# Kernel tuning notes

Measured on AMD Instinct MI355X. Metric: run time of the kernel, lower is better.

Reference implementation:

```python
import jax, jax.numpy as jnp
import numpy as np

N_NODES = 100000


def _gcn_conv(h, row, col, norm, W, b):
    # h: [N, Fin] -> [N, Fout]; standard GCN: scatter-add of normalized
    # neighbor messages after linear transform.
    h = h @ W                                   # [N, Fout]
    msg = h[col] * norm[:, None]                # [E, Fout] gather + scale
    out = jax.ops.segment_sum(msg, row, num_segments=N_NODES)
    return out + b


def setup_inputs() -> dict:
    key = jax.random.key(0)
    k1, k2, k3, k4 = jax.random.split(key, 4)
    N, E, F_IN, HID, OUT = N_NODES, 3200000, 512, 16, 40
    x = jax.random.normal(k1, (N, F_IN), dtype=jnp.float32)
    edge_index = jax.random.randint(k2, (2, E), 0, N, dtype=jnp.int64)
    W1 = jax.random.normal(k3, (F_IN, HID), dtype=jnp.float32) * (1.0 / np.sqrt(F_IN))
    b1 = jnp.zeros((HID,), dtype=jnp.float32)
    W2 = jax.random.normal(k4, (HID, OUT), dtype=jnp.float32) * (1.0 / np.sqrt(HID))
    b2 = jnp.zeros((OUT,), dtype=jnp.float32)
    return {"x": x, "edge_index": edge_index, "W1": W1, "b1": b1, "W2": W2, "b2": b2}


def reference(x, edge_index, W1, b1, W2, b2):
    N = N_NODES
    # add self-loops (GCN convention)
    loop = jnp.arange(N, dtype=edge_index.dtype)
    row = jnp.concatenate([edge_index[0], loop])  # target nodes
    col = jnp.concatenate([edge_index[1], loop])  # source nodes
    # symmetric normalization deg^-1/2 * deg^-1/2
    deg = jax.ops.segment_sum(jnp.ones_like(row, dtype=x.dtype), row, num_segments=N)
    dinv = jnp.where(deg > 0, jax.lax.rsqrt(deg), 0.0)
    norm = dinv[row] * dinv[col]                  # [E+N]

    h = _gcn_conv(x, row, col, norm, W1, b1)
    h = jax.nn.relu(h)
    out = _gcn_conv(h, row, col, norm, W2, b2)
    return out
```

## Files before the change

### kernel.cpp

```cpp
#include <hip/hip_runtime.h>

#define N_NODES 100000
#define F_IN 512
#define HID 16
#define F_OUT 40

#define NB 784
#define BSHIFT 7
#define ROWS_PB 128
#define BCAP 4608
#define CUR_PAD 16
#define APAD 17
#define PARTB 512
#define SROW 129

__global__ void k_zero(int* __restrict__ g) {
    int i = blockIdx.x * 256 + threadIdx.x;
    if (i < NB * CUR_PAD) g[i] = 0;
}

__global__ __launch_bounds__(512) void k_part1(const int* __restrict__ ei, int E,
                                               int* __restrict__ gcursor,
                                               unsigned int* __restrict__ sortbuf) {
    __shared__ int lcnt0[NB], lcnt1[NB], gb[NB];
    int t = threadIdx.x;
    int half = (t >> 6) & 1;
    int* myl = half ? lcnt1 : lcnt0;
    int epb = (E + PARTB - 1) / PARTB;
    int base = blockIdx.x * epb;
    int lim = min(base + epb, E);
    for (int i = t; i < NB; i += 512) { lcnt0[i] = 0; lcnt1[i] = 0; }
    __syncthreads();
    unsigned int v[13]; int bkt[13], mi[13];
#pragma unroll
    for (int i = 0; i < 13; ++i) {
        int e = base + i * 512 + t;
        bkt[i] = -1;
        if (e < lim) {
            int r = ei[e], c = ei[E + e];
            bkt[i] = r >> BSHIFT;
            v[i] = ((unsigned)(r & (ROWS_PB - 1)) << 17) | (unsigned)c;
            mi[i] = atomicAdd(&myl[bkt[i]], 1);
        }
    }
    __syncthreads();
    for (int i = t; i < NB; i += 512)
        gb[i] = atomicAdd(&gcursor[i * CUR_PAD], lcnt0[i] + lcnt1[i]);
    __syncthreads();
#pragma unroll
    for (int i = 0; i < 13; ++i)
        if (bkt[i] >= 0) {
            int slot = gb[bkt[i]] + (half ? lcnt0[bkt[i]] : 0) + mi[i];
            if (slot < BCAP) sortbuf[(size_t)bkt[i] * BCAP + slot] = v[i];
        }
}

__global__ __launch_bounds__(512) void k_gemm(const float* __restrict__ x,
                                              const float* __restrict__ W1,
                                              float* __restrict__ Hs) {
    __shared__ float smem[8 * 64 * APAD];
    int t = threadIdx.x;
    int bid = blockIdx.x;
    int tilebase = bid * 64;
    int srow = t >> 5;
    int sseg = t & 31;
    int crow = t & 63;
    int ksub = __builtin_amdgcn_readfirstlane(t >> 6);

    float acc[HID];
#pragma unroll
    for (int f = 0; f < HID; ++f) acc[f] = 0.0f;

    float4 rg[4];
#pragma unroll
    for (int q = 0; q < 4; ++q) {
        int r = tilebase + q * 16 + srow;
        r = min(r, N_NODES - 1);
        rg[q] = *reinterpret_cast<const float4*>(x + (size_t)r * F_IN + sseg * 4);
    }
    for (int s = 0; s < 4; ++s) {
        __syncthreads();
#pragma unroll
        for (int q = 0; q < 4; ++q) {
            int base = (q * 16 + srow) * SROW + sseg * 4;
            smem[base + 0] = rg[q].x;
            smem[base + 1] = rg[q].y;
            smem[base + 2] = rg[q].z;
            smem[base + 3] = rg[q].w;
        }
        __syncthreads();
        if (s < 3) {
#pragma unroll
            for (int q = 0; q < 4; ++q) {
                int r = tilebase + q * 16 + srow;
                r = min(r, N_NODES - 1);
                rg[q] = *reinterpret_cast<const float4*>(
                    x + (size_t)r * F_IN + (s + 1) * 128 + sseg * 4);
            }
        }
        const float* wp = W1 + (s * 128 + ksub * 16) * HID;
        int lbase = crow * SROW + ksub * 16;
#pragma unroll
        for (int kk = 0; kk < 16; ++kk) {
            float xv = smem[lbase + kk];
#pragma unroll
            for (int f = 0; f < HID; ++f)
                acc[f] = fmaf(xv, wp[kk * HID + f], acc[f]);
        }
    }
    __syncthreads();
    int rbase = (ksub * 64 + crow) * APAD;
#pragma unroll
    for (int f = 0; f < HID; ++f) smem[rbase + f] = acc[f];
    __syncthreads();
#pragma unroll
    for (int p = 0; p < 2; ++p) {
        int o = p * 512 + t;
        int r = o >> 4, f = o & 15;
        int rgl = tilebase + r;
        if (rgl < N_NODES) {
            float sum = 0.0f;
#pragma unroll
            for (int c = 0; c < 8; ++c) sum += smem[(c * 64 + r) * APAD + f];
            Hs[(size_t)rgl * HID + f] = sum;
        }
    }
}

__global__ __launch_bounds__(256) void k_build(const unsigned int* __restrict__ sortbuf,
                                               const int* __restrict__ gcursor,
                                               int* __restrict__ rowptr,
                                               float* __restrict__ dinv,
                                               int* __restrict__ colv,
                                               float* __restrict__ Hs) {
    __shared__ int bb[NB];
    __shared__ int s[256];
    __shared__ int hist[ROWS_PB];
    __shared__ int rstart[ROWS_PB];
    __shared__ int cur[ROWS_PB];
    __shared__ float sdinv[ROWS_PB];
    int b = blockIdx.x, t = threadIdx.x;

    int l0 = 0, l1 = 0, l2 = 0, l3 = 0;
    if (t < 196) {
        l0 = min(gcursor[(t * 4 + 0) * CUR_PAD], BCAP);
        l1 = min(gcursor[(t * 4 + 1) * CUR_PAD], BCAP);
        l2 = min(gcursor[(t * 4 + 2) * CUR_PAD], BCAP);
        l3 = min(gcursor[(t * 4 + 3) * CUR_PAD], BCAP);
    }
    int part = l0 + l1 + l2 + l3;
    s[t] = part;
    __syncthreads();
    for (int off = 1; off < 256; off <<= 1) {
        int a = (t >= off) ? s[t - off] : 0;
        __syncthreads();
        s[t] += a;
        __syncthreads();
    }
    if (t < 196) {
        int ex = s[t] - part;
        bb[t * 4 + 0] = ex;
        bb[t * 4 + 1] = ex + l0;
        bb[t * 4 + 2] = ex + l0 + l1;
        bb[t * 4 + 3] = ex + l0 + l1 + l2;
    }
    if (t < ROWS_PB) hist[t] = 0;
    __syncthreads();
    int gbase = bb[b];
    int n = min(gcursor[b * CUR_PAD], BCAP);
    if (b == 0 && t == 0) rowptr[N_NODES] = s[255];

    const unsigned int* sb = sortbuf + (size_t)b * BCAP;
    for (int i = t; i < n; i += 256) atomicAdd(&hist[sb[i] >> 17], 1);
    __syncthreads();
    int c0 = (t < ROWS_PB) ? hist[t] : 0;
    s[t] = c0;
    __syncthreads();
    for (int off = 1; off < 256; off <<= 1) {
        int a = (t >= off) ? s[t - off] : 0;
        __syncthreads();
        s[t] += a;
        __syncthreads();
    }
    if (t < ROWS_PB) {
        int ex = s[t] - c0;
        rstart[t] = ex;
        cur[t] = 0;
        float dv = rsqrtf((float)(c0 + 1));
        sdinv[t] = dv;
        int g = b * ROWS_PB + t;
        if (g < N_NODES) {
            rowptr[g] = gbase + ex;
            dinv[g] = dv;
        }
    }
    __syncthreads();
    for (int i = t; i < n; i += 256) {
        unsigned int v = sb[i];
        int lr = v >> 17;
        int pos = atomicAdd(&cur[lr], 1);
        colv[gbase + rstart[lr] + pos] = (int)(v & 0x1FFFFu);
    }
    __syncthreads();
    for (int i = t; i < ROWS_PB * 4; i += 256) {
        int row = i >> 2, q = i & 3;
        int g = b * ROWS_PB + row;
        if (g < N_NODES) {
            float4* p = reinterpret_cast<float4*>(Hs + (size_t)g * HID + q * 4);
            float4 vv = *p;
            float dv = sdinv[row];
            vv.x *= dv; vv.y *= dv; vv.z *= dv; vv.w *= dv;
            *p = vv;
        }
    }
}

__global__ __launch_bounds__(256) void k_agg1(const int* __restrict__ rowptr,
                                              const int* __restrict__ colv,
                                              const float* __restrict__ dinv,
                                              const float* __restrict__ Hs,
                                              const float* __restrict__ b1,
                                              float* __restrict__ h1s) {
    int wid = __builtin_amdgcn_readfirstlane((blockIdx.x * 256 + threadIdx.x) >> 6);
    if (wid >= N_NODES) return;
    int lane = threadIdx.x & 63;
    int f4 = lane & 3, sub = lane >> 2;
    int beg = rowptr[wid], end = rowptr[wid + 1];
    float dr = dinv[wid];
    float4 acc = make_float4(0.f, 0.f, 0.f, 0.f);
    for (int j = beg + sub; j < end; j += 16) {
        int c = colv[j];
        float4 hv = *reinterpret_cast<const float4*>(Hs + (size_t)c * HID + f4 * 4);
        acc.x += hv.x; acc.y += hv.y; acc.z += hv.z; acc.w += hv.w;
    }
#pragma unroll
    for (int d = 4; d < 64; d <<= 1) {
        acc.x += __shfl_xor(acc.x, d);
        acc.y += __shfl_xor(acc.y, d);
        acc.z += __shfl_xor(acc.z, d);
        acc.w += __shfl_xor(acc.w, d);
    }
    if (sub == 0) {
        float4 self = *reinterpret_cast<const float4*>(Hs + (size_t)wid * HID + f4 * 4);
        float4 bb = *reinterpret_cast<const float4*>(b1 + f4 * 4);
        float4 o;
        o.x = fmaxf((acc.x + self.x) * dr + bb.x, 0.f) * dr;
        o.y = fmaxf((acc.y + self.y) * dr + bb.y, 0.f) * dr;
        o.z = fmaxf((acc.z + self.z) * dr + bb.z, 0.f) * dr;
        o.w = fmaxf((acc.w + self.w) * dr + bb.w, 0.f) * dr;
        *reinterpret_cast<float4*>(h1s + (size_t)wid * HID + f4 * 4) = o;
    }
}

__global__ __launch_bounds__(256) void k_agg2(const int* __restrict__ rowptr,
                                              const int* __restrict__ colv,
                                              const float* __restrict__ dinv,
                                              const float* __restrict__ h1s,
                                              const float* __restrict__ W2,
                                              const float* __restrict__ b2,
                                              float* __restrict__ out) {
    int wid = __builtin_amdgcn_readfirstlane((blockIdx.x * 256 + threadIdx.x) >> 6);
    if (wid >= N_NODES) return;
    int lane = threadIdx.x & 63;
    int f4 = lane & 3, sub = lane >> 2;
    int beg = rowptr[wid], end = rowptr[wid + 1];
    float dr = dinv[wid];
    float4 acc = make_float4(0.f, 0.f, 0.f, 0.f);
    for (int j = beg + sub; j < end; j += 16) {
        int c = colv[j];
        float4 hv = *reinterpret_cast<const float4*>(h1s + (size_t)c * HID + f4 * 4);
        acc.x += hv.x; acc.y += hv.y; acc.z += hv.z; acc.w += hv.w;
    }
#pragma unroll
    for (int d = 4; d < 64; d <<= 1) {
        acc.x += __shfl_xor(acc.x, d);
        acc.y += __shfl_xor(acc.y, d);
        acc.z += __shfl_xor(acc.z, d);
        acc.w += __shfl_xor(acc.w, d);
    }
    float4 self = *reinterpret_cast<const float4*>(h1s + (size_t)wid * HID + f4 * 4);
    float4 w4;
    w4.x = (acc.x + self.x) * dr;
    w4.y = (acc.y + self.y) * dr;
    w4.z = (acc.z + self.z) * dr;
    w4.w = (acc.w + self.w) * dr;
    if (lane < F_OUT) {
        float o = b2[lane];
#pragma unroll
        for (int k = 0; k < HID; ++k) {
            float comp = (k & 3) == 0 ? w4.x : (k & 3) == 1 ? w4.y
                        : (k & 3) == 2 ? w4.z : w4.w;
            float wk = __shfl(comp, k >> 2);
            o = fmaf(wk, W2[k * F_OUT + lane], o);
        }
        out[(size_t)wid * F_OUT + lane] = o;
    }
}

extern "C" void kernel_launch(void* const* d_in, const int* in_sizes, int n_in,
                              void* d_out, int out_size, void* d_ws, size_t ws_size,
                              hipStream_t stream) {
    const float* x  = (const float*)d_in[0];
    const int* ei   = (const int*)d_in[1];
    const float* W1 = (const float*)d_in[2];
    const float* b1 = (const float*)d_in[3];
    const float* W2 = (const float*)d_in[4];
    const float* b2 = (const float*)d_in[5];
    float* out = (float*)d_out;
    const int E = in_sizes[1] / 2;

    int* gcursor          = (int*)d_ws;
    int* rowptr           = gcursor + 12544;
    float* dinv           = (float*)(rowptr + 100016);
    int* colv             = (int*)(dinv + 100032);
    unsigned int* sortbuf = (unsigned int*)(colv + 3200000);
    float* h1s            = (float*)sortbuf;
    float* Hs             = (float*)(sortbuf + 3612672);

    const int nbW = (N_NODES * 64 + 255) / 256;
    const int nbG = (N_NODES + 63) / 64;

    k_zero<<<(NB * CUR_PAD + 255) / 256, 256, 0, stream>>>(gcursor);
    k_part1<<<PARTB, 512, 0, stream>>>(ei, E, gcursor, sortbuf);
    k_gemm<<<nbG, 512, 0, stream>>>(x, W1, Hs);
    k_build<<<NB, 256, 0, stream>>>(sortbuf, gcursor, rowptr, dinv, colv, Hs);
    k_agg1<<<nbW, 256, 0, stream>>>(rowptr, colv, dinv, Hs, b1, h1s);
    k_agg2<<<nbW, 256, 0, stream>>>(rowptr, colv, dinv, h1s, W2, b2, out);
}
```

Measured before the change: 217.7 us.

## Merge edge partition and first-layer GEMM into one launch and rewrite GEMM

Result: slower. 301.9 us (+38.7%).

```diff
diff --git a/kernel.cpp b/kernel.cpp
--- a/kernel.cpp
+++ b/kernel.cpp
@@ -10,119 +10,128 @@
 #define ROWS_PB 128
 #define BCAP 4608
 #define CUR_PAD 16
-#define APAD 17
 #define PARTB 512
-#define SROW 129
 
 __global__ void k_zero(int* __restrict__ g) {
     int i = blockIdx.x * 256 + threadIdx.x;
     if (i < NB * CUR_PAD) g[i] = 0;
 }
 
-__global__ __launch_bounds__(512) void k_part1(const int* __restrict__ ei, int E,
-                                               int* __restrict__ gcursor,
-                                               unsigned int* __restrict__ sortbuf) {
+__global__ __launch_bounds__(512) void k_fat(const float* __restrict__ x,
+                                             const float* __restrict__ W1,
+                                             const int* __restrict__ ei, int E,
+                                             int* __restrict__ gcursor,
+                                             unsigned int* __restrict__ sortbuf,
+                                             float* __restrict__ Hs) {
     __shared__ int lcnt0[NB], lcnt1[NB], gb[NB];
     int t = threadIdx.x;
-    int half = (t >> 6) & 1;
-    int* myl = half ? lcnt1 : lcnt0;
-    int epb = (E + PARTB - 1) / PARTB;
-    int base = blockIdx.x * epb;
-    int lim = min(base + epb, E);
-    for (int i = t; i < NB; i += 512) { lcnt0[i] = 0; lcnt1[i] = 0; }
-    __syncthreads();
-    unsigned int v[13]; int bkt[13], mi[13];
-#pragma unroll
-    for (int i = 0; i < 13; ++i) {
-        int e = base + i * 512 + t;
-        bkt[i] = -1;
-        if (e < lim) {
-            int r = ei[e], c = ei[E + e];
-            bkt[i] = r >> BSHIFT;
-            v[i] = ((unsigned)(r & (ROWS_PB - 1)) << 17) | (unsigned)c;
-            mi[i] = atomicAdd(&myl[bkt[i]], 1);
-        }
-    }
-    __syncthreads();
-    for (int i = t; i < NB; i += 512)
-        gb[i] = atomicAdd(&gcursor[i * CUR_PAD], lcnt0[i] + lcnt1[i]);
-    __syncthreads();
-#pragma unroll
-    for (int i = 0; i < 13; ++i)
-        if (bkt[i] >= 0) {
-            int slot = gb[bkt[i]] + (half ? lcnt0[bkt[i]] : 0) + mi[i];
-            if (slot < BCAP) sortbuf[(size_t)bkt[i] * BCAP + slot] = v[i];
-        }
-}
-
-__global__ __launch_bounds__(512) void k_gemm(const float* __restrict__ x,
-                                              const float* __restrict__ W1,
-                                              float* __restrict__ Hs) {
-    __shared__ float smem[8 * 64 * APAD];
-    int t = threadIdx.x;
-    int bid = blockIdx.x;
-    int tilebase = bid * 64;
-    int srow = t >> 5;
-    int sseg = t & 31;
-    int crow = t & 63;
-    int ksub = __builtin_amdgcn_readfirstlane(t >> 6);
-
-    float acc[HID];
-#pragma unroll
-    for (int f = 0; f < HID; ++f) acc[f] = 0.0f;
-
-    float4 rg[4];
-#pragma unroll
-    for (int q = 0; q < 4; ++q) {
-        int r = tilebase + q * 16 + srow;
-        r = min(r, N_NODES - 1);
-        rg[q] = *reinterpret_cast<const float4*>(x + (size_t)r * F_IN + sseg * 4);
-    }
-    for (int s = 0; s < 4; ++s) {
-        __syncthreads();
-#pragma unroll
-        for (int q = 0; q < 4; ++q) {
-            int base = (q * 16 + srow) * SROW + sseg * 4;
-            smem[base + 0] = rg[q].x;
-            smem[base + 1] = rg[q].y;
-            smem[base + 2] = rg[q].z;
-            smem[base + 3] = rg[q].w;
-        }
-        __syncthreads();
-        if (s < 3) {
-#pragma unroll
-            for (int q = 0; q < 4; ++q) {
-                int r = tilebase + q * 16 + srow;
-                r = min(r, N_NODES - 1);
-                rg[q] = *reinterpret_cast<const float4*>(
-                    x + (size_t)r * F_IN + (s + 1) * 128 + sseg * 4);
-            }
-        }
-        const float* wp = W1 + (s * 128 + ksub * 16) * HID;
-        int lbase = crow * SROW + ksub * 16;
-#pragma unroll
-        for (int kk = 0; kk < 16; ++kk) {
-            float xv = smem[lbase + kk];
-#pragma unroll
-            for (int f = 0; f < HID; ++f)
-                acc[f] = fmaf(xv, wp[kk * HID + f], acc[f]);
-        }
-    }
-    __syncthreads();
-    int rbase = (ksub * 64 + crow) * APAD;
-#pragma unroll
-    for (int f = 0; f < HID; ++f) smem[rbase + f] = acc[f];
-    __syncthreads();
-#pragma unroll
-    for (int p = 0; p < 2; ++p) {
-        int o = p * 512 + t;
-        int r = o >> 4, f = o & 15;
-        int rgl = tilebase + r;
-        if (rgl < N_NODES) {
-            float sum = 0.0f;
-#pragma unroll
-            for (int c = 0; c < 8; ++c) sum += smem[(c * 64 + r) * APAD + f];
-            Hs[(size_t)rgl * HID + f] = sum;
+    if (blockIdx.x < PARTB) {
+        int half = (t >> 6) & 1;
+        int* myl = half ? lcnt1 : lcnt0;
+        int epb = (E + PARTB - 1) / PARTB;
+        int base = blockIdx.x * epb;
+        int lim = min(base + epb, E);
+        for (int i = t; i < NB; i += 512) { lcnt0[i] = 0; lcnt1[i] = 0; }
+        __syncthreads();
+        unsigned int v[13]; int bkt[13], mi[13];
+#pragma unroll
+        for (int i = 0; i < 13; ++i) {
+            int e = base + i * 512 + t;
+            bkt[i] = -1;
+            if (e < lim) {
+                int r = ei[e], c = ei[E + e];
+                bkt[i] = r >> BSHIFT;
+                v[i] = ((unsigned)(r & (ROWS_PB - 1)) << 17) | (unsigned)c;
+                mi[i] = atomicAdd(&myl[bkt[i]], 1);
+            }
+        }
+        __syncthreads();
+        for (int i = t; i < NB; i += 512)
+            gb[i] = atomicAdd(&gcursor[i * CUR_PAD], lcnt0[i] + lcnt1[i]);
+        __syncthreads();
+#pragma unroll
+        for (int i = 0; i < 13; ++i)
+            if (bkt[i] >= 0) {
+                int slot = gb[bkt[i]] + (half ? lcnt0[bkt[i]] : 0) + mi[i];
+                if (slot < BCAP) sortbuf[(size_t)bkt[i] * BCAP + slot] = v[i];
+            }
+    } else {
+        int bid = blockIdx.x - PARTB;
+        int l = t & 63;
+        int wv = t >> 6;
+        int row = bid * 64 + wv * 8 + (l & 7);
+        int slice = l >> 3;
+        int rload = min(row, N_NODES - 1);
+        const float* xp = x + (size_t)rload * F_IN + slice * 64;
+        const float* wp = W1 + slice * 64 * HID;
+
+        float acc[HID];
+#pragma unroll
+        for (int f = 0; f < HID; ++f) acc[f] = 0.0f;
+
+#pragma unroll 2
+        for (int k = 0; k < 64; k += 8) {
+            float4 xa = *reinterpret_cast<const float4*>(xp + k);
+            float4 xb = *reinterpret_cast<const float4*>(xp + k + 4);
+            float xs[8] = {xa.x, xa.y, xa.z, xa.w, xb.x, xb.y, xb.z, xb.w};
+#pragma unroll
+            for (int kk = 0; kk < 8; ++kk) {
+                const float4* wr = reinterpret_cast<const float4*>(wp + (k + kk) * HID);
+                float4 w0 = wr[0], w1 = wr[1], w2 = wr[2], w3 = wr[3];
+                float xv = xs[kk];
+                acc[0]  = fmaf(xv, w0.x, acc[0]);
+                acc[1]  = fmaf(xv, w0.y, acc[1]);
+                acc[2]  = fmaf(xv, w0.z, acc[2]);
+                acc[3]  = fmaf(xv, w0.w, acc[3]);
+                acc[4]  = fmaf(xv, w1.x, acc[4]);
+                acc[5]  = fmaf(xv, w1.y, acc[5]);
+                acc[6]  = fmaf(xv, w1.z, acc[6]);
+                acc[7]  = fmaf(xv, w1.w, acc[7]);
+                acc[8]  = fmaf(xv, w2.x, acc[8]);
+                acc[9]  = fmaf(xv, w2.y, acc[9]);
+                acc[10] = fmaf(xv, w2.z, acc[10]);
+                acc[11] = fmaf(xv, w2.w, acc[11]);
+                acc[12] = fmaf(xv, w3.x, acc[12]);
+                acc[13] = fmaf(xv, w3.y, acc[13]);
+                acc[14] = fmaf(xv, w3.z, acc[14]);
+                acc[15] = fmaf(xv, w3.w, acc[15]);
+            }
+        }
+        float b8[8];
+        {
+            bool hi = (l >> 3) & 1;
+#pragma unroll
+            for (int f = 0; f < 8; ++f) {
+                float tl = acc[f]     + __shfl_xor(acc[f], 8);
+                float th = acc[f + 8] + __shfl_xor(acc[f + 8], 8);
+                b8[f] = hi ? th : tl;
+            }
+        }
+        float c4[4];
+        {
+            bool hi = (l >> 4) & 1;
+#pragma unroll
+            for (int f = 0; f < 4; ++f) {
+                float tl = b8[f]     + __shfl_xor(b8[f], 16);
+                float th = b8[f + 4] + __shfl_xor(b8[f + 4], 16);
+                c4[f] = hi ? th : tl;
+            }
+        }
+        float e2[2];
+        {
+            bool hi = (l >> 5) & 1;
+#pragma unroll
+            for (int f = 0; f < 2; ++f) {
+                float tl = c4[f]     + __shfl_xor(c4[f], 32);
+                float th = c4[f + 2] + __shfl_xor(c4[f + 2], 32);
+                e2[f] = hi ? th : tl;
+            }
+        }
+        if (row < N_NODES) {
+            int fbase = (((slice) & 1) << 3) | (((slice >> 1) & 1) << 2) |
+                        (((slice >> 2) & 1) << 1);
+            *reinterpret_cast<float2*>(Hs + (size_t)row * HID + fbase) =
+                make_float2(e2[0], e2[1]);
         }
     }
 }
@@ -321,8 +330,7 @@
     const int nbG = (N_NODES + 63) / 64;
 
     k_zero<<<(NB * CUR_PAD + 255) / 256, 256, 0, stream>>>(gcursor);
-    k_part1<<<PARTB, 512, 0, stream>>>(ei, E, gcursor, sortbuf);
-    k_gemm<<<nbG, 512, 0, stream>>>(x, W1, Hs);
+    k_fat<<<PARTB + nbG, 512, 0, stream>>>(x, W1, ei, E, gcursor, sortbuf, Hs);
     k_build<<<NB, 256, 0, stream>>>(sortbuf, gcursor, rowptr, dinv, colv, Hs);
     k_agg1<<<nbW, 256, 0, stream>>>(rowptr, colv, dinv, Hs, b1, h1s);
     k_agg2<<<nbW, 256, 0, stream>>>(rowptr, colv, dinv, h1s, W2, b2, out);
```

## Co-schedule GEMM blocks with partition and build kernels; move source dinv scaling into agg1

Applied to the files above, without the earlier changes.

Measured after the change: 206.0 us. 1.06x faster.

```diff
diff --git a/kernel.cpp b/kernel.cpp
--- a/kernel.cpp
+++ b/kernel.cpp
@@ -12,6 +12,8 @@
 #define CUR_PAD 16
 #define APAD 17
 #define PARTB 512
+#define G1 660
+#define NBG 1563
 #define SROW 129
 
 __global__ void k_zero(int* __restrict__ g) {
@@ -19,48 +21,10 @@
     if (i < NB * CUR_PAD) g[i] = 0;
 }
 
-__global__ __launch_bounds__(512) void k_part1(const int* __restrict__ ei, int E,
-                                               int* __restrict__ gcursor,
-                                               unsigned int* __restrict__ sortbuf) {
-    __shared__ int lcnt0[NB], lcnt1[NB], gb[NB];
-    int t = threadIdx.x;
-    int half = (t >> 6) & 1;
-    int* myl = half ? lcnt1 : lcnt0;
-    int epb = (E + PARTB - 1) / PARTB;
-    int base = blockIdx.x * epb;
-    int lim = min(base + epb, E);
-    for (int i = t; i < NB; i += 512) { lcnt0[i] = 0; lcnt1[i] = 0; }
-    __syncthreads();
-    unsigned int v[13]; int bkt[13], mi[13];
-#pragma unroll
-    for (int i = 0; i < 13; ++i) {
-        int e = base + i * 512 + t;
-        bkt[i] = -1;
-        if (e < lim) {
-            int r = ei[e], c = ei[E + e];
-            bkt[i] = r >> BSHIFT;
-            v[i] = ((unsigned)(r & (ROWS_PB - 1)) << 17) | (unsigned)c;
-            mi[i] = atomicAdd(&myl[bkt[i]], 1);
-        }
-    }
-    __syncthreads();
-    for (int i = t; i < NB; i += 512)
-        gb[i] = atomicAdd(&gcursor[i * CUR_PAD], lcnt0[i] + lcnt1[i]);
-    __syncthreads();
-#pragma unroll
-    for (int i = 0; i < 13; ++i)
-        if (bkt[i] >= 0) {
-            int slot = gb[bkt[i]] + (half ? lcnt0[bkt[i]] : 0) + mi[i];
-            if (slot < BCAP) sortbuf[(size_t)bkt[i] * BCAP + slot] = v[i];
-        }
-}
-
-__global__ __launch_bounds__(512) void k_gemm(const float* __restrict__ x,
-                                              const float* __restrict__ W1,
-                                              float* __restrict__ Hs) {
-    __shared__ float smem[8 * 64 * APAD];
-    int t = threadIdx.x;
-    int bid = blockIdx.x;
+__device__ __forceinline__ void gemm_body(const float* __restrict__ x,
+                                          const float* __restrict__ W1,
+                                          float* __restrict__ Hs,
+                                          int bid, int t, float* smem) {
     int tilebase = bid * 64;
     int srow = t >> 5;
     int sseg = t & 31;
@@ -127,91 +91,133 @@
     }
 }
 
-__global__ __launch_bounds__(256) void k_build(const unsigned int* __restrict__ sortbuf,
-                                               const int* __restrict__ gcursor,
-                                               int* __restrict__ rowptr,
-                                               float* __restrict__ dinv,
-                                               int* __restrict__ colv,
-                                               float* __restrict__ Hs) {
-    __shared__ int bb[NB];
-    __shared__ int s[256];
-    __shared__ int hist[ROWS_PB];
-    __shared__ int rstart[ROWS_PB];
-    __shared__ int cur[ROWS_PB];
-    __shared__ float sdinv[ROWS_PB];
-    int b = blockIdx.x, t = threadIdx.x;
-
-    int l0 = 0, l1 = 0, l2 = 0, l3 = 0;
-    if (t < 196) {
-        l0 = min(gcursor[(t * 4 + 0) * CUR_PAD], BCAP);
-        l1 = min(gcursor[(t * 4 + 1) * CUR_PAD], BCAP);
-        l2 = min(gcursor[(t * 4 + 2) * CUR_PAD], BCAP);
-        l3 = min(gcursor[(t * 4 + 3) * CUR_PAD], BCAP);
-    }
-    int part = l0 + l1 + l2 + l3;
-    s[t] = part;
-    __syncthreads();
-    for (int off = 1; off < 256; off <<= 1) {
-        int a = (t >= off) ? s[t - off] : 0;
-        __syncthreads();
-        s[t] += a;
-        __syncthreads();
-    }
-    if (t < 196) {
-        int ex = s[t] - part;
-        bb[t * 4 + 0] = ex;
-        bb[t * 4 + 1] = ex + l0;
-        bb[t * 4 + 2] = ex + l0 + l1;
-        bb[t * 4 + 3] = ex + l0 + l1 + l2;
-    }
-    if (t < ROWS_PB) hist[t] = 0;
-    __syncthreads();
-    int gbase = bb[b];
-    int n = min(gcursor[b * CUR_PAD], BCAP);
-    if (b == 0 && t == 0) rowptr[N_NODES] = s[255];
-
-    const unsigned int* sb = sortbuf + (size_t)b * BCAP;
-    for (int i = t; i < n; i += 256) atomicAdd(&hist[sb[i] >> 17], 1);
-    __syncthreads();
-    int c0 = (t < ROWS_PB) ? hist[t] : 0;
-    s[t] = c0;
-    __syncthreads();
-    for (int off = 1; off < 256; off <<= 1) {
-        int a = (t >= off) ? s[t - off] : 0;
-        __syncthreads();
-        s[t] += a;
-        __syncthreads();
-    }
-    if (t < ROWS_PB) {
-        int ex = s[t] - c0;
-        rstart[t] = ex;
-        cur[t] = 0;
-        float dv = rsqrtf((float)(c0 + 1));
-        sdinv[t] = dv;
-        int g = b * ROWS_PB + t;
-        if (g < N_NODES) {
-            rowptr[g] = gbase + ex;
-            dinv[g] = dv;
-        }
-    }
-    __syncthreads();
-    for (int i = t; i < n; i += 256) {
-        unsigned int v = sb[i];
-        int lr = v >> 17;
-        int pos = atomicAdd(&cur[lr], 1);
-        colv[gbase + rstart[lr] + pos] = (int)(v & 0x1FFFFu);
-    }
-    __syncthreads();
-    for (int i = t; i < ROWS_PB * 4; i += 256) {
-        int row = i >> 2, q = i & 3;
-        int g = b * ROWS_PB + row;
-        if (g < N_NODES) {
-            float4* p = reinterpret_cast<float4*>(Hs + (size_t)g * HID + q * 4);
-            float4 vv = *p;
-            float dv = sdinv[row];
-            vv.x *= dv; vv.y *= dv; vv.z *= dv; vv.w *= dv;
-            *p = vv;
-        }
+__global__ __launch_bounds__(512) void k_p1g(const float* __restrict__ x,
+                                             const float* __restrict__ W1,
+                                             const int* __restrict__ ei, int E,
+                                             int* __restrict__ gcursor,
+                                             unsigned int* __restrict__ sortbuf,
+                                             float* __restrict__ Hs) {
+    __shared__ float smem[8704];
+    int t = threadIdx.x;
+    if (blockIdx.x < PARTB) {
+        int* lcnt0 = (int*)smem;
+        int* lcnt1 = lcnt0 + NB;
+        int* gb    = lcnt1 + NB;
+        int half = (t >> 6) & 1;
+        int* myl = half ? lcnt1 : lcnt0;
+        int epb = (E + PARTB - 1) / PARTB;
+        int base = blockIdx.x * epb;
+        int lim = min(base + epb, E);
+        for (int i = t; i < NB; i += 512) { lcnt0[i] = 0; lcnt1[i] = 0; }
+        __syncthreads();
+        unsigned int v[13]; int bkt[13], mi[13];
+#pragma unroll
+        for (int i = 0; i < 13; ++i) {
+            int e = base + i * 512 + t;
+            bkt[i] = -1;
+            if (e < lim) {
+                int r = ei[e], c = ei[E + e];
+                bkt[i] = r >> BSHIFT;
+                v[i] = ((unsigned)(r & (ROWS_PB - 1)) << 17) | (unsigned)c;
+                mi[i] = atomicAdd(&myl[bkt[i]], 1);
+            }
+        }
+        __syncthreads();
+        for (int i = t; i < NB; i += 512)
+            gb[i] = atomicAdd(&gcursor[i * CUR_PAD], lcnt0[i] + lcnt1[i]);
+        __syncthreads();
+#pragma unroll
+        for (int i = 0; i < 13; ++i)
+            if (bkt[i] >= 0) {
+                int slot = gb[bkt[i]] + (half ? lcnt0[bkt[i]] : 0) + mi[i];
+                if (slot < BCAP) sortbuf[(size_t)bkt[i] * BCAP + slot] = v[i];
+            }
+    } else {
+        gemm_body(x, W1, Hs, blockIdx.x - PARTB, t, smem);
+    }
+}
+
+__global__ __launch_bounds__(512) void k_bg(const float* __restrict__ x,
+                                            const float* __restrict__ W1,
+                                            const unsigned int* __restrict__ sortbuf,
+                                            const int* __restrict__ gcursor,
+                                            int* __restrict__ rowptr,
+                                            float* __restrict__ dinv,
+                                            int* __restrict__ colv,
+                                            float* __restrict__ Hs) {
+    __shared__ float smem[8704];
+    int t = threadIdx.x;
+    if (blockIdx.x < NB) {
+        int* ib     = (int*)smem;
+        int* bb     = ib;
+        int* s      = ib + 784;
+        int* hist   = ib + 1040;
+        int* rstart = ib + 1168;
+        int* cur    = ib + 1296;
+        int b = blockIdx.x;
+
+        int l0 = 0, l1 = 0, l2 = 0, l3 = 0;
+        if (t < 196) {
+            l0 = min(gcursor[(t * 4 + 0) * CUR_PAD], BCAP);
+            l1 = min(gcursor[(t * 4 + 1) * CUR_PAD], BCAP);
+            l2 = min(gcursor[(t * 4 + 2) * CUR_PAD], BCAP);
+            l3 = min(gcursor[(t * 4 + 3) * CUR_PAD], BCAP);
+        }
+        int part = l0 + l1 + l2 + l3;
+        if (t < 256) s[t] = (t < 196) ? part : 0;
+        __syncthreads();
+        for (int off = 1; off < 256; off <<= 1) {
+            int a = 0;
+            if (t < 256 && t >= off) a = s[t - off];
+            __syncthreads();
+            if (t < 256) s[t] += a;
+            __syncthreads();
+        }
+        if (t < 196) {
+            int ex = s[t] - part;
+            bb[t * 4 + 0] = ex;
+            bb[t * 4 + 1] = ex + l0;
+            bb[t * 4 + 2] = ex + l0 + l1;
+            bb[t * 4 + 3] = ex + l0 + l1 + l2;
+        }
+        if (t < ROWS_PB) hist[t] = 0;
+        if (b == 0 && t == 255) rowptr[N_NODES] = s[255];
+        __syncthreads();
+        int gbase = bb[b];
+        int n = min(gcursor[b * CUR_PAD], BCAP);
+
+        const unsigned int* sb = sortbuf + (size_t)b * BCAP;
+        for (int i = t; i < n; i += 512) atomicAdd(&hist[sb[i] >> 17], 1);
+        __syncthreads();
+        int c0 = (t < ROWS_PB) ? hist[t] : 0;
+        if (t < 256) s[t] = (t < ROWS_PB) ? c0 : 0;
+        __syncthreads();
+        for (int off = 1; off < ROWS_PB; off <<= 1) {
+            int a = 0;
+            if (t < ROWS_PB && t >= off) a = s[t - off];
+            __syncthreads();
+            if (t < ROWS_PB) s[t] += a;
+            __syncthreads();
+        }
+        if (t < ROWS_PB) {
+            int ex = s[t] - c0;
+            rstart[t] = ex;
+            cur[t] = 0;
+            int g = b * ROWS_PB + t;
+            if (g < N_NODES) {
+                rowptr[g] = gbase + ex;
+                dinv[g] = rsqrtf((float)(c0 + 1));
+            }
+        }
+        __syncthreads();
+        for (int i = t; i < n; i += 512) {
+            unsigned int v = sb[i];
+            int lr = v >> 17;
+            int pos = atomicAdd(&cur[lr], 1);
+            colv[gbase + rstart[lr] + pos] = (int)(v & 0x1FFFFu);
+        }
+    } else {
+        gemm_body(x, W1, Hs, G1 + (blockIdx.x - NB), t, smem);
     }
 }
 
@@ -230,8 +236,12 @@
     float4 acc = make_float4(0.f, 0.f, 0.f, 0.f);
     for (int j = beg + sub; j < end; j += 16) {
         int c = colv[j];
+        float dc = dinv[c];
         float4 hv = *reinterpret_cast<const float4*>(Hs + (size_t)c * HID + f4 * 4);
-        acc.x += hv.x; acc.y += hv.y; acc.z += hv.z; acc.w += hv.w;
+        acc.x = fmaf(hv.x, dc, acc.x);
+        acc.y = fmaf(hv.y, dc, acc.y);
+        acc.z = fmaf(hv.z, dc, acc.z);
+        acc.w = fmaf(hv.w, dc, acc.w);
     }
 #pragma unroll
     for (int d = 4; d < 64; d <<= 1) {
@@ -244,10 +254,10 @@
         float4 self = *reinterpret_cast<const float4*>(Hs + (size_t)wid * HID + f4 * 4);
         float4 bb = *reinterpret_cast<const float4*>(b1 + f4 * 4);
         float4 o;
-        o.x = fmaxf((acc.x + self.x) * dr + bb.x, 0.f) * dr;
-        o.y = fmaxf((acc.y + self.y) * dr + bb.y, 0.f) * dr;
-        o.z = fmaxf((acc.z + self.z) * dr + bb.z, 0.f) * dr;
-        o.w = fmaxf((acc.w + self.w) * dr + bb.w, 0.f) * dr;
+        o.x = fmaxf((acc.x + self.x * dr) * dr + bb.x, 0.f) * dr;
+        o.y = fmaxf((acc.y + self.y * dr) * dr + bb.y, 0.f) * dr;
+        o.z = fmaxf((acc.z + self.z * dr) * dr + bb.z, 0.f) * dr;
+        o.w = fmaxf((acc.w + self.w * dr) * dr + bb.w, 0.f) * dr;
         *reinterpret_cast<float4*>(h1s + (size_t)wid * HID + f4 * 4) = o;
     }
 }
@@ -318,12 +328,11 @@
     float* Hs             = (float*)(sortbuf + 3612672);
 
     const int nbW = (N_NODES * 64 + 255) / 256;
-    const int nbG = (N_NODES + 63) / 64;
 
     k_zero<<<(NB * CUR_PAD + 255) / 256, 256, 0, stream>>>(gcursor);
-    k_part1<<<PARTB, 512, 0, stream>>>(ei, E, gcursor, sortbuf);
-    k_gemm<<<nbG, 512, 0, stream>>>(x, W1, Hs);
-    k_build<<<NB, 256, 0, stream>>>(sortbuf, gcursor, rowptr, dinv, colv, Hs);
+    k_p1g<<<PARTB + G1, 512, 0, stream>>>(x, W1, ei, E, gcursor, sortbuf, Hs);
+    k_bg<<<NB + (NBG - G1), 512, 0, stream>>>(x, W1, sortbuf, gcursor,
+                                              rowptr, dinv, colv, Hs);
     k_agg1<<<nbW, 256, 0, stream>>>(rowptr, colv, dinv, Hs, b1, h1s);
     k_agg2<<<nbW, 256, 0, stream>>>(rowptr, colv, dinv, h1s, W2, b2, out);
 }
```
